# Kernel tuning notes

Measured on AMD Instinct MI355X. Metric: run time of the kernel, lower is better.

## Reference

```python
import jax, jax.numpy as jnp
import numpy as np

D_MODEL = 2048
NUM_HEADS = 16
HEAD_DIM = 128
ROPE_BASE = 10000.0
NEG_INF = -1e9


def setup_inputs() -> dict:
    key = jax.random.key(0)
    ks = jax.random.split(key, 5)
    B, S = 2, 2048
    hidden_states = jax.random.normal(ks[0], (B, S, D_MODEL), dtype=jnp.float32)
    # additive causal mask: 0 on/below diagonal, large-negative above
    causal = jnp.triu(jnp.full((S, S), NEG_INF, dtype=jnp.float32), k=1)
    attention_mask = jnp.broadcast_to(causal, (B, 1, S, S))
    position_ids = jnp.broadcast_to(jnp.arange(S, dtype=jnp.int32), (B, S))
    scale = 1.0 / np.sqrt(D_MODEL)
    Wq = jax.random.normal(ks[1], (D_MODEL, NUM_HEADS * HEAD_DIM), dtype=jnp.float32) * scale
    Wk = jax.random.normal(ks[2], (D_MODEL, NUM_HEADS * HEAD_DIM), dtype=jnp.float32) * scale
    Wv = jax.random.normal(ks[3], (D_MODEL, NUM_HEADS * HEAD_DIM), dtype=jnp.float32) * scale
    Wo = jax.random.normal(ks[4], (NUM_HEADS * HEAD_DIM, D_MODEL), dtype=jnp.float32) * scale
    return {"hidden_states": hidden_states, "attention_mask": attention_mask,
            "position_ids": position_ids, "Wq": Wq, "Wk": Wk, "Wv": Wv, "Wo": Wo}


def _rope_cos_sin(position_ids):
    # inv_freq: [head_dim/2]
    inv_freq = 1.0 / (ROPE_BASE ** (jnp.arange(0, HEAD_DIM, 2, dtype=jnp.float32) / HEAD_DIM))
    freqs = position_ids.astype(jnp.float32)[..., None] * inv_freq  # [B,S,hd/2]
    emb = jnp.concatenate([freqs, freqs], axis=-1)  # [B,S,hd]
    return jnp.cos(emb), jnp.sin(emb)


def _rotate_half(x):
    x1, x2 = jnp.split(x, 2, axis=-1)
    return jnp.concatenate([-x2, x1], axis=-1)


def reference(hidden_states, attention_mask, position_ids, Wq, Wk, Wv, Wo):
    B, S, _ = hidden_states.shape
    H, Dh = NUM_HEADS, HEAD_DIM
    q = (hidden_states @ Wq).reshape(B, S, H, Dh).transpose(0, 2, 1, 3)  # [B,H,S,Dh]
    k = (hidden_states @ Wk).reshape(B, S, H, Dh).transpose(0, 2, 1, 3)
    v = (hidden_states @ Wv).reshape(B, S, H, Dh).transpose(0, 2, 1, 3)
    cos, sin = _rope_cos_sin(position_ids)  # [B,S,Dh]
    cos = cos[:, None, :, :]  # [B,1,S,Dh]
    sin = sin[:, None, :, :]
    q = q * cos + _rotate_half(q) * sin
    k = k * cos + _rotate_half(k) * sin
    scaling = 1.0 / np.sqrt(Dh)
    scores = jnp.einsum('bhqd,bhkd->bhqk', q, k) * scaling  # [B,H,S,S]
    scores = scores + attention_mask[:, :, :, :S]
    attn = jax.nn.softmax(scores.astype(jnp.float32), axis=-1).astype(q.dtype)
    # dropout p=0.0 / eval mode -> identity
    out = jnp.einsum('bhqk,bhkd->bhqd', attn, v)  # [B,H,S,Dh]
    out = out.transpose(0, 2, 1, 3).reshape(B, S, H * Dh)
    return out @ Wo
```

## Files before the change

kernel.cpp:

```cpp
#include <hip/hip_runtime.h>

typedef __attribute__((ext_vector_type(4))) float f32x4;
typedef __attribute__((ext_vector_type(8))) _Float16 f16x8;
typedef __attribute__((ext_vector_type(4))) _Float16 f16x4;

#define SEQ 2048
#define DM 2048
#define NQKV 6144

__device__ __forceinline__ void gload16(const _Float16* g, _Float16* l) {
  __builtin_amdgcn_global_load_lds(
      (const __attribute__((address_space(1))) void*)g,
      (__attribute__((address_space(3))) void*)l, 16, 0, 0);
}

__global__ __launch_bounds__(256) void cvt_x_kernel(const float* __restrict__ X,
                                                    _Float16* __restrict__ Xb, int n4) {
  int i = blockIdx.x * 256 + threadIdx.x;
  if (i < n4) {
    const float4 v = ((const float4*)X)[i];
    f16x4 o;
    o.x = (_Float16)v.x; o.y = (_Float16)v.y; o.z = (_Float16)v.z; o.w = (_Float16)v.w;
    ((f16x4*)Xb)[i] = o;
  }
}

__global__ __launch_bounds__(256) void wtrans_all_kernel(const float* __restrict__ Wq,
                                                         const float* __restrict__ Wk,
                                                         const float* __restrict__ Wv,
                                                         const float* __restrict__ Wo,
                                                         _Float16* __restrict__ Wqkvt,
                                                         _Float16* __restrict__ Wot) {
  __shared__ float tile[32][33];
  const int z = blockIdx.z;
  const float* W = (z == 0) ? Wq : (z == 1) ? Wk : (z == 2) ? Wv : Wo;
  _Float16* Wt = (z < 3) ? (Wqkvt + (size_t)z * 2048 * 2048) : Wot;
  const int n0 = blockIdx.x * 32, k0 = blockIdx.y * 32;
  const int tx = threadIdx.x & 31, ty = threadIdx.x >> 5;
#pragma unroll
  for (int i = 0; i < 32; i += 8)
    tile[ty + i][tx] = W[(size_t)(k0 + ty + i) * 2048 + n0 + tx];
  __syncthreads();
#pragma unroll
  for (int i = 0; i < 32; i += 8)
    Wt[(size_t)(n0 + ty + i) * 2048 + k0 + tx] = (_Float16)tile[tx][ty + i];
}

__global__ __launch_bounds__(256) void rope_table_kernel(float* __restrict__ ct,
                                                         float* __restrict__ st) {
  int i = blockIdx.x * 256 + threadIdx.x;
  int pos = i >> 6, f = i & 63;
  float inv = powf(10000.0f, -(float)f / 64.0f);
  float ang = (float)pos * inv;
  ct[i] = cosf(ang);
  st[i] = sinf(ang);
}

template <bool OUTF32>
__global__ __launch_bounds__(512, 2) void gemm8n_kernel(const _Float16* __restrict__ A,
                                                        const _Float16* __restrict__ Bt,
                                                        void* __restrict__ Cout,
                                                        int M, int N, int K) {
  __shared__ __align__(16) _Float16 As[3 * 16384];
  __shared__ __align__(16) _Float16 Bs[3 * 8192];
  const int nwg = gridDim.x * gridDim.y;
  const int orig = blockIdx.y * gridDim.x + blockIdx.x;
  const int id = (orig & 7) * (nwg >> 3) + (orig >> 3);
  const int bx = id % gridDim.x, by = id / gridDim.x;
  const int bm = by * 256, bn = bx * 128;
  const int t = threadIdx.x, lane = t & 63, w = t >> 6;
  const int wm = w >> 2, wn = w & 3;
  const int rl = lane & 15, lr4 = lane >> 4;
  const int NKT = K >> 6;

  const int srow = t >> 3;
  const int scol = ((t & 7) ^ (srow & 7)) << 3;
  const _Float16* pA = A + (size_t)(bm + srow) * K + scol;
  const _Float16* pB = Bt + (size_t)(bn + srow) * K + scol;
  _Float16* lA = As + t * 8;
  _Float16* lB = Bs + t * 8;
  const size_t rowK64 = (size_t)64 * K;

#define STA(H, KT, SLOT)                                                   \
  { const size_t _g = (size_t)((H) * 128) * K + (size_t)(KT) * 64;         \
    gload16(pA + _g, lA + (SLOT) * 16384 + (H) * 8192);                    \
    gload16(pA + _g + rowK64, lA + (SLOT) * 16384 + (H) * 8192 + 4096); }
#define STB(KT, SLOT)                                                      \
  { const size_t _g = (size_t)(KT) * 64;                                   \
    gload16(pB + _g, lB + (SLOT) * 8192);                                  \
    gload16(pB + _g + rowK64, lB + (SLOT) * 8192 + 4096); }

  const int sw0 = (lr4 ^ (rl & 7)) << 3;
  const int sw1 = ((4 + lr4) ^ (rl & 7)) << 3;
  const int aoff = (wm * 64 + rl) * 64;
  const int boff = (wn * 32 + rl) * 64;

  f16x8 a_[4][2], b_[2][2];
  f32x4 acc[2][4][2];
#pragma unroll
  for (int qm = 0; qm < 2; ++qm)
#pragma unroll
    for (int mf = 0; mf < 4; ++mf)
#pragma unroll
      for (int nf = 0; nf < 2; ++nf) acc[qm][mf][nf] = (f32x4)0.0f;

#define LOAD_A(H, SLOT)                                                 \
  { const _Float16* _p = As + (SLOT) * 16384 + (H) * 8192 + aoff;       \
    _Pragma("unroll") for (int mf = 0; mf < 4; ++mf) {                  \
      a_[mf][0] = *(const f16x8*)&_p[mf * 1024 + sw0];                  \
      a_[mf][1] = *(const f16x8*)&_p[mf * 1024 + sw1]; } }
#define LOAD_B(SLOT)                                                    \
  { const _Float16* _p = Bs + (SLOT) * 8192 + boff;                     \
    _Pragma("unroll") for (int nf = 0; nf < 2; ++nf) {                  \
      b_[nf][0] = *(const f16x8*)&_p[nf * 1024 + sw0];                  \
      b_[nf][1] = *(const f16x8*)&_p[nf * 1024 + sw1]; } }
#define MFMA_Q(QM)                                                      \
  __builtin_amdgcn_s_setprio(1);                                        \
  _Pragma("unroll") for (int mf = 0; mf < 4; ++mf)                      \
    _Pragma("unroll") for (int nf = 0; nf < 2; ++nf) {                  \
      acc[QM][mf][nf] = __builtin_amdgcn_mfma_f32_16x16x32_f16(         \
          a_[mf][0], b_[nf][0], acc[QM][mf][nf], 0, 0, 0);              \
      acc[QM][mf][nf] = __builtin_amdgcn_mfma_f32_16x16x32_f16(         \
          a_[mf][1], b_[nf][1], acc[QM][mf][nf], 0, 0, 0); }            \
  __builtin_amdgcn_s_setprio(0);
#define BAR()                                                           \
  do { __builtin_amdgcn_sched_barrier(0); __builtin_amdgcn_s_barrier(); \
       __builtin_amdgcn_sched_barrier(0); } while (0)
#define LGKM0()                                                         \
  do { asm volatile("s_waitcnt lgkmcnt(0)" ::: "memory");               \
       __builtin_amdgcn_sched_barrier(0); } while (0)
#define VM6() asm volatile("s_waitcnt vmcnt(6)" ::: "memory")
#define VM0() asm volatile("s_waitcnt vmcnt(0)" ::: "memory")

  STA(0, 0, 0); STB(0, 0); STA(1, 0, 0);
  STA(0, 1, 1); STB(1, 1); STA(1, 1, 1);
  VM6();
  BAR();

  for (int jb = 0; jb + 4 < NKT; jb += 3) {
    LOAD_A(0, 0); LOAD_B(0); STA(0, jb + 2, 2); STB(jb + 2, 2);
    BAR(); LGKM0(); MFMA_Q(0); BAR();
    LOAD_A(1, 0); STA(1, jb + 2, 2);
    VM6(); BAR(); LGKM0(); MFMA_Q(1); BAR();
    LOAD_A(0, 1); LOAD_B(1); STA(0, jb + 3, 0); STB(jb + 3, 0);
    BAR(); LGKM0(); MFMA_Q(0); BAR();
    LOAD_A(1, 1); STA(1, jb + 3, 0);
    VM6(); BAR(); LGKM0(); MFMA_Q(1); BAR();
    LOAD_A(0, 2); LOAD_B(2); STA(0, jb + 4, 1); STB(jb + 4, 1);
    BAR(); LGKM0(); MFMA_Q(0); BAR();
    LOAD_A(1, 2); STA(1, jb + 4, 1);
    VM6(); BAR(); LGKM0(); MFMA_Q(1); BAR();
  }
  {
    LOAD_A(0, 0); LOAD_B(0);
    BAR(); LGKM0(); MFMA_Q(0); BAR();
    LOAD_A(1, 0);
    VM0();
    BAR(); LGKM0(); MFMA_Q(1); BAR();
    LOAD_A(0, 1); LOAD_B(1);
    BAR(); LGKM0(); MFMA_Q(0); BAR();
    LOAD_A(1, 1);
    BAR(); LGKM0(); MFMA_Q(1);
  }

#pragma unroll
  for (int qm = 0; qm < 2; ++qm)
#pragma unroll
    for (int mf = 0; mf < 4; ++mf)
#pragma unroll
      for (int nf = 0; nf < 2; ++nf) {
        const int col = bn + wn * 32 + nf * 16 + rl;
#pragma unroll
        for (int ri = 0; ri < 4; ++ri) {
          const int row = bm + qm * 128 + wm * 64 + mf * 16 + lr4 * 4 + ri;
          if (OUTF32)
            ((float*)Cout)[(size_t)row * N + col] = acc[qm][mf][nf][ri];
          else
            ((_Float16*)Cout)[(size_t)row * N + col] = (_Float16)acc[qm][mf][nf][ri];
        }
      }
#undef STA
#undef STB
#undef LOAD_A
#undef LOAD_B
#undef MFMA_Q
#undef BAR
#undef LGKM0
#undef VM6
#undef VM0
}

__global__ __launch_bounds__(256) void rope_qk_kernel(const _Float16* __restrict__ QKVo,
                                                      const int* __restrict__ pos_ids,
                                                      const float* __restrict__ ct,
                                                      const float* __restrict__ st,
                                                      _Float16* __restrict__ Q,
                                                      _Float16* __restrict__ K) {
  int id = blockIdx.x * 256 + threadIdx.x;
  int f = id & 63;
  int h = (id >> 6) & 15;
  int s_ = (id >> 10) & 2047;
  int b = (id >> 21) & 1;
  int row = b * SEQ + s_;
  int pos = pos_ids[row];
  float c = ct[pos * 64 + f], sn = st[pos * 64 + f];
  size_t base = (size_t)row * NQKV;
  float q1 = (float)QKVo[base + h * 128 + f];
  float q2 = (float)QKVo[base + h * 128 + f + 64];
  float k1 = (float)QKVo[base + 2048 + h * 128 + f];
  float k2 = (float)QKVo[base + 2048 + h * 128 + f + 64];
  const float scale = 0.08838834764831845f;
  size_t obase = (((size_t)(b * 16 + h)) * SEQ + s_) * 128;
  Q[obase + f]      = (_Float16)((q1 * c - q2 * sn) * scale);
  Q[obase + f + 64] = (_Float16)((q2 * c + q1 * sn) * scale);
  K[obase + f]      = (_Float16)(k1 * c - k2 * sn);
  K[obase + f + 64] = (_Float16)(k2 * c + k1 * sn);
}

__global__ __launch_bounds__(256) void v_transpose_kernel(const _Float16* __restrict__ QKVo,
                                                          _Float16* __restrict__ Vt) {
  __shared__ _Float16 tile[32][40];
  const int s0 = blockIdx.x * 32, d0 = blockIdx.y * 32, bh = blockIdx.z;
  const int b = bh >> 4, h = bh & 15;
  const int tx = threadIdx.x & 31, ty = threadIdx.x >> 5;
#pragma unroll
  for (int i = 0; i < 32; i += 8) {
    int s_ = s0 + ty + i;
    tile[ty + i][tx] = QKVo[(size_t)(b * SEQ + s_) * NQKV + 4096 + h * 128 + d0 + tx];
  }
  __syncthreads();
#pragma unroll
  for (int i = 0; i < 32; i += 8) {
    int d = d0 + ty + i;
    Vt[((size_t)bh * 128 + d) * SEQ + s0 + tx] = tile[tx][ty + i];
  }
}

__global__ __launch_bounds__(512) void attn_kernel(const _Float16* __restrict__ Q,
                                                   const _Float16* __restrict__ K,
                                                   const _Float16* __restrict__ Vt,
                                                   _Float16* __restrict__ O) {
  __shared__ __align__(16) _Float16 Ks[2][64 * 128];
  __shared__ __align__(16) _Float16 Vs[2][128 * 64];
  __shared__ __align__(16) _Float16 Ps[8][16 * 72];
  const int bh = blockIdx.x;
  const int pair = blockIdx.y;
  const int b = bh >> 4, h = bh & 15;
  const int t = threadIdx.x, lane = t & 63, w = t >> 6;
  const int lr = lane >> 4, lc = lane & 15;
  const _Float16* Qb = Q + (size_t)bh * SEQ * 128;
  const _Float16* Kb = K + (size_t)bh * SEQ * 128;
  const _Float16* Vb = Vt + (size_t)bh * 128 * SEQ;

  auto stage = [&](int buf, int kb) {
    const int k0 = kb * 64;
#pragma unroll
    for (int i = 0; i < 2; ++i) {
      const int c = i * 512 + t;
      const int row = c >> 4, u = c & 15;
      gload16(&Kb[(size_t)(k0 + row) * 128 + ((u ^ (row & 7)) * 8)], &Ks[buf][c * 8]);
    }
#pragma unroll
    for (int i = 0; i < 2; ++i) {
      const int c = i * 512 + t;
      const int dim = c >> 3, u = c & 7;
      gload16(&Vb[(size_t)dim * SEQ + k0 + ((u ^ (dim & 7)) * 8)], &Vs[buf][c * 8]);
    }
  };

  for (int half = 0; half < 2; ++half) {
    const int j = half ? (15 - pair) : pair;
    const int q0 = j * 128;
    const int nkb = 2 * j + 2;
    const int rowmin = q0 + w * 16;

    f16x8 qf[4];
    {
      const int qrow = q0 + w * 16 + lc;
#pragma unroll
      for (int kk = 0; kk < 4; ++kk)
        qf[kk] = *(const f16x8*)&Qb[(size_t)qrow * 128 + kk * 32 + lr * 8];
    }
    f32x4 acco[8];
#pragma unroll
    for (int i = 0; i < 8; ++i) acco[i] = (f32x4)0.0f;
    float m_r[4] = {-1e30f, -1e30f, -1e30f, -1e30f};
    float l_r[4] = {0.f, 0.f, 0.f, 0.f};

    stage(0, 0);
    __syncthreads();
    for (int kb = 0; kb < nkb; ++kb) {
      const int cur = kb & 1;
      if (kb + 1 < nkb) stage(cur ^ 1, kb + 1);
      const int k0 = kb * 64;
      if (k0 <= rowmin + 15) {
        f32x4 sacc[4];
#pragma unroll
        for (int jj = 0; jj < 4; ++jj) sacc[jj] = (f32x4)0.0f;
#pragma unroll
        for (int jj = 0; jj < 4; ++jj) {
          const int krow = jj * 16 + lc;
#pragma unroll
          for (int kk = 0; kk < 4; ++kk) {
            const int idx = (krow * 128 + kk * 32 + lr * 8) ^ ((krow & 7) << 3);
            f16x8 kf = *(const f16x8*)&Ks[cur][idx];
            sacc[jj] = __builtin_amdgcn_mfma_f32_16x16x32_f16(qf[kk], kf, sacc[jj], 0, 0, 0);
          }
        }
        const bool diag = (k0 + 63 > rowmin);
#pragma unroll
        for (int r = 0; r < 4; ++r) {
          const int rowi = rowmin + lr * 4 + r;
          float s[4], mx = -1e30f;
#pragma unroll
          for (int jj = 0; jj < 4; ++jj) {
            float sv = sacc[jj][r];
            if (diag && (k0 + jj * 16 + lc > rowi)) sv = -1e30f;
            s[jj] = sv;
            mx = fmaxf(mx, sv);
          }
#pragma unroll
          for (int msk = 1; msk < 16; msk <<= 1) mx = fmaxf(mx, __shfl_xor(mx, msk));
          const float mn = fmaxf(m_r[r], mx);
          const float sc = __expf(m_r[r] - mn);
          float rs = 0.f;
#pragma unroll
          for (int jj = 0; jj < 4; ++jj) {
            float pv = __expf(s[jj] - mn);
            rs += pv;
            Ps[w][(lr * 4 + r) * 72 + jj * 16 + lc] = (_Float16)pv;
          }
#pragma unroll
          for (int msk = 1; msk < 16; msk <<= 1) rs += __shfl_xor(rs, msk);
          l_r[r] = l_r[r] * sc + rs;
          m_r[r] = mn;
#pragma unroll
          for (int tt = 0; tt < 8; ++tt) acco[tt][r] *= sc;
        }
#pragma unroll
        for (int tt = 0; tt < 8; ++tt) {
          const int dim = tt * 16 + lc;
#pragma unroll
          for (int ch = 0; ch < 2; ++ch) {
            f16x8 pf = *(const f16x8*)&Ps[w][lc * 72 + ch * 32 + lr * 8];
            const int vidx = (dim * 64 + ch * 32 + lr * 8) ^ ((dim & 7) << 3);
            f16x8 vf = *(const f16x8*)&Vs[cur][vidx];
            acco[tt] = __builtin_amdgcn_mfma_f32_16x16x32_f16(pf, vf, acco[tt], 0, 0, 0);
          }
        }
      }
      __syncthreads();
    }
#pragma unroll
    for (int tt = 0; tt < 8; ++tt) {
      const int col = h * 128 + tt * 16 + lc;
#pragma unroll
      for (int r = 0; r < 4; ++r) {
        const int row = q0 + w * 16 + lr * 4 + r;
        O[(size_t)(b * SEQ + row) * DM + col] = (_Float16)(acco[tt][r] / l_r[r]);
      }
    }
  }
}

extern "C" void kernel_launch(void* const* d_in, const int* in_sizes, int n_in,
                              void* d_out, int out_size, void* d_ws, size_t ws_size,
                              hipStream_t stream) {
  const float* hidden = (const float*)d_in[0];
  const int* pos_ids = (const int*)d_in[2];
  const float* Wq = (const float*)d_in[3];
  const float* Wk = (const float*)d_in[4];
  const float* Wv = (const float*)d_in[5];
  const float* Wo = (const float*)d_in[6];

  char* ws = (char*)d_ws;
  _Float16* Xb    = (_Float16*)(ws + 0);
  _Float16* Wqkvt = (_Float16*)(ws + 16777216);
  _Float16* Wot   = (_Float16*)(ws + 41943040);
  _Float16* QKVo  = (_Float16*)(ws + 50331648);
  _Float16* Kbuf  = (_Float16*)(ws + 100663296);
  float* ct       = (float*)(ws + 117440512);
  float* st       = (float*)(ws + 117964800);
  _Float16* Vtbuf = Xb;
  _Float16* Qbuf  = Wqkvt;
  _Float16* Obuf  = QKVo;

  cvt_x_kernel<<<8192, 256, 0, stream>>>(hidden, Xb, 2097152);
  wtrans_all_kernel<<<dim3(64, 64, 4), 256, 0, stream>>>(Wq, Wk, Wv, Wo, Wqkvt, Wot);
  rope_table_kernel<<<512, 256, 0, stream>>>(ct, st);

  gemm8n_kernel<false><<<dim3(48, 16), 512, 0, stream>>>(Xb, Wqkvt, QKVo, 4096, 6144, 2048);

  rope_qk_kernel<<<16384, 256, 0, stream>>>(QKVo, pos_ids, ct, st, Qbuf, Kbuf);
  v_transpose_kernel<<<dim3(64, 4, 32), 256, 0, stream>>>(QKVo, Vtbuf);

  attn_kernel<<<dim3(32, 8), 512, 0, stream>>>(Qbuf, Kbuf, Vtbuf, Obuf);

  gemm8n_kernel<true><<<dim3(16, 16), 512, 0, stream>>>(Obuf, Wot, d_out, 4096, 2048, 2048);
}
```

Measured before the change: 296.0 us.

## Read V directly from global, add lazy softmax rescale, raise occupancy hint

```diff
diff --git a/kernel.cpp b/kernel.cpp
--- a/kernel.cpp
+++ b/kernel.cpp
@@ -236,12 +236,11 @@
   }
 }
 
-__global__ __launch_bounds__(512) void attn_kernel(const _Float16* __restrict__ Q,
-                                                   const _Float16* __restrict__ K,
-                                                   const _Float16* __restrict__ Vt,
-                                                   _Float16* __restrict__ O) {
+__global__ __launch_bounds__(512, 4) void attn_kernel(const _Float16* __restrict__ Q,
+                                                      const _Float16* __restrict__ K,
+                                                      const _Float16* __restrict__ Vt,
+                                                      _Float16* __restrict__ O) {
   __shared__ __align__(16) _Float16 Ks[2][64 * 128];
-  __shared__ __align__(16) _Float16 Vs[2][128 * 64];
   __shared__ __align__(16) _Float16 Ps[8][16 * 72];
   const int bh = blockIdx.x;
   const int pair = blockIdx.y;
@@ -252,7 +251,7 @@
   const _Float16* Kb = K + (size_t)bh * SEQ * 128;
   const _Float16* Vb = Vt + (size_t)bh * 128 * SEQ;
 
-  auto stage = [&](int buf, int kb) {
+  auto stageK = [&](int buf, int kb) {
     const int k0 = kb * 64;
 #pragma unroll
     for (int i = 0; i < 2; ++i) {
@@ -260,12 +259,6 @@
       const int row = c >> 4, u = c & 15;
       gload16(&Kb[(size_t)(k0 + row) * 128 + ((u ^ (row & 7)) * 8)], &Ks[buf][c * 8]);
     }
-#pragma unroll
-    for (int i = 0; i < 2; ++i) {
-      const int c = i * 512 + t;
-      const int dim = c >> 3, u = c & 7;
-      gload16(&Vb[(size_t)dim * SEQ + k0 + ((u ^ (dim & 7)) * 8)], &Vs[buf][c * 8]);
-    }
   };
 
   for (int half = 0; half < 2; ++half) {
@@ -287,11 +280,11 @@
     float m_r[4] = {-1e30f, -1e30f, -1e30f, -1e30f};
     float l_r[4] = {0.f, 0.f, 0.f, 0.f};
 
-    stage(0, 0);
+    stageK(0, 0);
     __syncthreads();
     for (int kb = 0; kb < nkb; ++kb) {
       const int cur = kb & 1;
-      if (kb + 1 < nkb) stage(cur ^ 1, kb + 1);
+      if (kb + 1 < nkb) stageK(cur ^ 1, kb + 1);
       const int k0 = kb * 64;
       if (k0 <= rowmin + 15) {
         f32x4 sacc[4];
@@ -308,43 +301,66 @@
           }
         }
         const bool diag = (k0 + 63 > rowmin);
+        float mx[4];
 #pragma unroll
         for (int r = 0; r < 4; ++r) {
           const int rowi = rowmin + lr * 4 + r;
-          float s[4], mx = -1e30f;
+          float m0 = -1e30f;
 #pragma unroll
           for (int jj = 0; jj < 4; ++jj) {
             float sv = sacc[jj][r];
             if (diag && (k0 + jj * 16 + lc > rowi)) sv = -1e30f;
-            s[jj] = sv;
-            mx = fmaxf(mx, sv);
+            sacc[jj][r] = sv;
+            m0 = fmaxf(m0, sv);
           }
 #pragma unroll
-          for (int msk = 1; msk < 16; msk <<= 1) mx = fmaxf(mx, __shfl_xor(mx, msk));
-          const float mn = fmaxf(m_r[r], mx);
-          const float sc = __expf(m_r[r] - mn);
-          float rs = 0.f;
-#pragma unroll
-          for (int jj = 0; jj < 4; ++jj) {
-            float pv = __expf(s[jj] - mn);
-            rs += pv;
-            Ps[w][(lr * 4 + r) * 72 + jj * 16 + lc] = (_Float16)pv;
+          for (int msk = 1; msk < 16; msk <<= 1) m0 = fmaxf(m0, __shfl_xor(m0, msk));
+          mx[r] = m0;
+        }
+        bool needv = false;
+#pragma unroll
+        for (int r = 0; r < 4; ++r) needv |= (mx[r] > m_r[r] + 8.0f);
+        if (__any(needv)) {
+#pragma unroll
+          for (int r = 0; r < 4; ++r) {
+            const float mn = fmaxf(m_r[r], mx[r]);
+            const float sc = __expf(m_r[r] - mn);
+            float rs = 0.f;
+#pragma unroll
+            for (int jj = 0; jj < 4; ++jj) {
+              float pv = __expf(sacc[jj][r] - mn);
+              rs += pv;
+              Ps[w][(lr * 4 + r) * 72 + jj * 16 + lc] = (_Float16)pv;
+            }
+#pragma unroll
+            for (int msk = 1; msk < 16; msk <<= 1) rs += __shfl_xor(rs, msk);
+            l_r[r] = l_r[r] * sc + rs;
+            m_r[r] = mn;
+#pragma unroll
+            for (int tt = 0; tt < 8; ++tt) acco[tt][r] *= sc;
           }
-#pragma unroll
-          for (int msk = 1; msk < 16; msk <<= 1) rs += __shfl_xor(rs, msk);
-          l_r[r] = l_r[r] * sc + rs;
-          m_r[r] = mn;
-#pragma unroll
-          for (int tt = 0; tt < 8; ++tt) acco[tt][r] *= sc;
+        } else {
+#pragma unroll
+          for (int r = 0; r < 4; ++r) {
+            float rs = 0.f;
+#pragma unroll
+            for (int jj = 0; jj < 4; ++jj) {
+              float pv = __expf(sacc[jj][r] - m_r[r]);
+              rs += pv;
+              Ps[w][(lr * 4 + r) * 72 + jj * 16 + lc] = (_Float16)pv;
+            }
+#pragma unroll
+            for (int msk = 1; msk < 16; msk <<= 1) rs += __shfl_xor(rs, msk);
+            l_r[r] += rs;
+          }
         }
 #pragma unroll
         for (int tt = 0; tt < 8; ++tt) {
-          const int dim = tt * 16 + lc;
+          const _Float16* vrow = &Vb[(size_t)(tt * 16 + lc) * SEQ + k0];
 #pragma unroll
           for (int ch = 0; ch < 2; ++ch) {
             f16x8 pf = *(const f16x8*)&Ps[w][lc * 72 + ch * 32 + lr * 8];
-            const int vidx = (dim * 64 + ch * 32 + lr * 8) ^ ((dim & 7) << 3);
-            f16x8 vf = *(const f16x8*)&Vs[cur][vidx];
+            f16x8 vf = *(const f16x8*)&vrow[ch * 32 + lr * 8];
             acco[tt] = __builtin_amdgcn_mfma_f32_16x16x32_f16(pf, vf, acco[tt], 0, 0, 0);
           }
         }
```

Result: slower. 496.0 us (+67.6%).

## Fuse RoPE and V transpose into QKV GEMM epilogue

Applied to the files above, without the earlier changes.

```diff
diff --git a/kernel.cpp b/kernel.cpp
--- a/kernel.cpp
+++ b/kernel.cpp
@@ -56,13 +56,16 @@
   st[i] = sinf(ang);
 }
 
-template <bool OUTF32>
-__global__ __launch_bounds__(512, 2) void gemm8n_kernel(const _Float16* __restrict__ A,
-                                                        const _Float16* __restrict__ Bt,
-                                                        void* __restrict__ Cout,
-                                                        int M, int N, int K) {
-  __shared__ __align__(16) _Float16 As[3 * 16384];
-  __shared__ __align__(16) _Float16 Bs[3 * 8192];
+template <int MODE>
+__global__ __launch_bounds__(512, 2) void gemm8n_kernel(
+    const _Float16* __restrict__ A, const _Float16* __restrict__ Bt,
+    float* __restrict__ Cout, int M, int N, int K,
+    const int* __restrict__ pos_ids, const float* __restrict__ ct,
+    const float* __restrict__ st, _Float16* __restrict__ Qo,
+    _Float16* __restrict__ Ko, _Float16* __restrict__ Vo) {
+  __shared__ __align__(16) char smem[147456];
+  _Float16* As = (_Float16*)smem;
+  _Float16* Bs = (_Float16*)(smem + 98304);
   const int nwg = gridDim.x * gridDim.y;
   const int orig = blockIdx.y * gridDim.x + blockIdx.x;
   const int id = (orig & 7) * (nwg >> 3) + (orig >> 3);
@@ -163,22 +166,78 @@
     BAR(); LGKM0(); MFMA_Q(1);
   }
 
-#pragma unroll
-  for (int qm = 0; qm < 2; ++qm)
-#pragma unroll
-    for (int mf = 0; mf < 4; ++mf)
-#pragma unroll
-      for (int nf = 0; nf < 2; ++nf) {
-        const int col = bn + wn * 32 + nf * 16 + rl;
-#pragma unroll
-        for (int ri = 0; ri < 4; ++ri) {
-          const int row = bm + qm * 128 + wm * 64 + mf * 16 + lr4 * 4 + ri;
-          if (OUTF32)
-            ((float*)Cout)[(size_t)row * N + col] = acc[qm][mf][nf][ri];
-          else
-            ((_Float16*)Cout)[(size_t)row * N + col] = (_Float16)acc[qm][mf][nf][ri];
+  if (MODE == 0) {
+#pragma unroll
+    for (int qm = 0; qm < 2; ++qm)
+#pragma unroll
+      for (int mf = 0; mf < 4; ++mf)
+#pragma unroll
+        for (int nf = 0; nf < 2; ++nf) {
+          const int col = bn + wn * 32 + nf * 16 + rl;
+#pragma unroll
+          for (int ri = 0; ri < 4; ++ri) {
+            const int row = bm + qm * 128 + wm * 64 + mf * 16 + lr4 * 4 + ri;
+            Cout[(size_t)row * N + col] = acc[qm][mf][nf][ri];
+          }
         }
+  } else {
+    const int ttype = bx >> 4;
+    const int hh = bx & 15;
+    if (ttype == 2) {
+#pragma unroll
+      for (int qm = 0; qm < 2; ++qm)
+#pragma unroll
+        for (int mf = 0; mf < 4; ++mf)
+#pragma unroll
+          for (int nf = 0; nf < 2; ++nf) {
+            const int d = wn * 32 + nf * 16 + rl;
+            const int s0 = bm + qm * 128 + wm * 64 + mf * 16 + lr4 * 4;
+            const int bb = s0 >> 11, ss = s0 & 2047;
+            f16x4 v4;
+#pragma unroll
+            for (int ri = 0; ri < 4; ++ri) v4[ri] = (_Float16)acc[qm][mf][nf][ri];
+            *(f16x4*)&Vo[((size_t)(bb * 16 + hh) * 128 + d) * SEQ + ss] = v4;
+          }
+    } else {
+      float* cl = (float*)smem;
+      LGKM0();
+      BAR();
+#pragma unroll
+      for (int qm = 0; qm < 2; ++qm)
+#pragma unroll
+        for (int mf = 0; mf < 4; ++mf)
+#pragma unroll
+          for (int nf = 0; nf < 2; ++nf) {
+            const int col = wn * 32 + nf * 16 + rl;
+            const int r0 = qm * 128 + wm * 64 + mf * 16 + lr4 * 4;
+#pragma unroll
+            for (int ri = 0; ri < 4; ++ri) cl[(r0 + ri) * 130 + col] = acc[qm][mf][nf][ri];
+          }
+      BAR();
+      const int row = t >> 1, pb = (t & 1) * 32;
+      const int rg = bm + row;
+      const int bb = rg >> 11, ss = rg & 2047;
+      const int pos = pos_ids[rg];
+      const float* cp = ct + pos * 64 + pb;
+      const float* sp = st + pos * 64 + pb;
+      _Float16* dst = (ttype ? Ko : Qo) + ((size_t)(bb * 16 + hh) * SEQ + ss) * 128;
+      const float qs = ttype ? 1.0f : 0.08838834764831845f;
+      const float* crow = cl + row * 130;
+      _Float16 o1[32], o2[32];
+#pragma unroll
+      for (int i = 0; i < 32; ++i) {
+        const float x1 = crow[pb + i], x2 = crow[pb + 64 + i];
+        const float c = cp[i], s = sp[i];
+        o1[i] = (_Float16)((x1 * c - x2 * s) * qs);
+        o2[i] = (_Float16)((x2 * c + x1 * s) * qs);
       }
+#pragma unroll
+      for (int i = 0; i < 4; ++i) {
+        *(f16x8*)&dst[pb + i * 8] = *(f16x8*)&o1[i * 8];
+        *(f16x8*)&dst[pb + 64 + i * 8] = *(f16x8*)&o2[i * 8];
+      }
+    }
+  }
 #undef STA
 #undef STB
 #undef LOAD_A
@@ -188,52 +247,6 @@
 #undef LGKM0
 #undef VM6
 #undef VM0
-}
-
-__global__ __launch_bounds__(256) void rope_qk_kernel(const _Float16* __restrict__ QKVo,
-                                                      const int* __restrict__ pos_ids,
-                                                      const float* __restrict__ ct,
-                                                      const float* __restrict__ st,
-                                                      _Float16* __restrict__ Q,
-                                                      _Float16* __restrict__ K) {
-  int id = blockIdx.x * 256 + threadIdx.x;
-  int f = id & 63;
-  int h = (id >> 6) & 15;
-  int s_ = (id >> 10) & 2047;
-  int b = (id >> 21) & 1;
-  int row = b * SEQ + s_;
-  int pos = pos_ids[row];
-  float c = ct[pos * 64 + f], sn = st[pos * 64 + f];
-  size_t base = (size_t)row * NQKV;
-  float q1 = (float)QKVo[base + h * 128 + f];
-  float q2 = (float)QKVo[base + h * 128 + f + 64];
-  float k1 = (float)QKVo[base + 2048 + h * 128 + f];
-  float k2 = (float)QKVo[base + 2048 + h * 128 + f + 64];
-  const float scale = 0.08838834764831845f;
-  size_t obase = (((size_t)(b * 16 + h)) * SEQ + s_) * 128;
-  Q[obase + f]      = (_Float16)((q1 * c - q2 * sn) * scale);
-  Q[obase + f + 64] = (_Float16)((q2 * c + q1 * sn) * scale);
-  K[obase + f]      = (_Float16)(k1 * c - k2 * sn);
-  K[obase + f + 64] = (_Float16)(k2 * c + k1 * sn);
-}
-
-__global__ __launch_bounds__(256) void v_transpose_kernel(const _Float16* __restrict__ QKVo,
-                                                          _Float16* __restrict__ Vt) {
-  __shared__ _Float16 tile[32][40];
-  const int s0 = blockIdx.x * 32, d0 = blockIdx.y * 32, bh = blockIdx.z;
-  const int b = bh >> 4, h = bh & 15;
-  const int tx = threadIdx.x & 31, ty = threadIdx.x >> 5;
-#pragma unroll
-  for (int i = 0; i < 32; i += 8) {
-    int s_ = s0 + ty + i;
-    tile[ty + i][tx] = QKVo[(size_t)(b * SEQ + s_) * NQKV + 4096 + h * 128 + d0 + tx];
-  }
-  __syncthreads();
-#pragma unroll
-  for (int i = 0; i < 32; i += 8) {
-    int d = d0 + ty + i;
-    Vt[((size_t)bh * 128 + d) * SEQ + s0 + tx] = tile[tx][ty + i];
-  }
 }
 
 __global__ __launch_bounds__(512) void attn_kernel(const _Float16* __restrict__ Q,
@@ -377,24 +390,23 @@
   _Float16* Xb    = (_Float16*)(ws + 0);
   _Float16* Wqkvt = (_Float16*)(ws + 16777216);
   _Float16* Wot   = (_Float16*)(ws + 41943040);
-  _Float16* QKVo  = (_Float16*)(ws + 50331648);
-  _Float16* Kbuf  = (_Float16*)(ws + 100663296);
+  _Float16* Qbuf  = (_Float16*)(ws + 50331648);
+  _Float16* Kbuf  = (_Float16*)(ws + 67108864);
+  _Float16* Vtbuf = (_Float16*)(ws + 83886080);
+  _Float16* Obuf  = (_Float16*)(ws + 100663296);
   float* ct       = (float*)(ws + 117440512);
   float* st       = (float*)(ws + 117964800);
-  _Float16* Vtbuf = Xb;
-  _Float16* Qbuf  = Wqkvt;
-  _Float16* Obuf  = QKVo;
 
   cvt_x_kernel<<<8192, 256, 0, stream>>>(hidden, Xb, 2097152);
   wtrans_all_kernel<<<dim3(64, 64, 4), 256, 0, stream>>>(Wq, Wk, Wv, Wo, Wqkvt, Wot);
   rope_table_kernel<<<512, 256, 0, stream>>>(ct, st);
 
-  gemm8n_kernel<false><<<dim3(48, 16), 512, 0, stream>>>(Xb, Wqkvt, QKVo, 4096, 6144, 2048);
-
-  rope_qk_kernel<<<16384, 256, 0, stream>>>(QKVo, pos_ids, ct, st, Qbuf, Kbuf);
-  v_transpose_kernel<<<dim3(64, 4, 32), 256, 0, stream>>>(QKVo, Vtbuf);
+  gemm8n_kernel<1><<<dim3(48, 16), 512, 0, stream>>>(
+      Xb, Wqkvt, nullptr, 4096, 6144, 2048, pos_ids, ct, st, Qbuf, Kbuf, Vtbuf);
 
   attn_kernel<<<dim3(32, 8), 512, 0, stream>>>(Qbuf, Kbuf, Vtbuf, Obuf);
 
-  gemm8n_kernel<true><<<dim3(16, 16), 512, 0, stream>>>(Obuf, Wot, d_out, 4096, 2048, 2048);
-}
+  gemm8n_kernel<0><<<dim3(16, 16), 512, 0, stream>>>(
+      Obuf, Wot, (float*)d_out, 4096, 2048, 2048, nullptr, nullptr, nullptr,
+      nullptr, nullptr, nullptr);
+}
```

Result: faster. 281.7 us (-4.8%).
